# Optimization experiments

Hardware: AMD Instinct MI355X
Metric: run time of the kernel (lower is better)

Reference implementation:

```python
import jax, jax.numpy as jnp
import numpy as np

N_NODES = 50000
IN_CH = 256
Z_DIM = 64
N_EDGES = 800000


def setup_inputs() -> dict:
    key = jax.random.key(0)
    k_x, k_e, k_wm, k_ws = jax.random.split(key, 4)
    x = jax.random.normal(k_x, (N_NODES, IN_CH), dtype=jnp.float32)
    edge_index = jax.random.randint(k_e, (2, N_EDGES), 0, N_NODES, dtype=jnp.int64)
    # Glorot-style init like PyG GCNConv
    scale = 1.0 / np.sqrt(IN_CH)
    W_mu = jax.random.uniform(k_wm, (IN_CH, Z_DIM), dtype=jnp.float32, minval=-scale, maxval=scale)
    W_logstd = jax.random.uniform(k_ws, (IN_CH, Z_DIM), dtype=jnp.float32, minval=-scale, maxval=scale)
    b_mu = jnp.zeros((Z_DIM,), dtype=jnp.float32)
    b_logstd = jnp.zeros((Z_DIM,), dtype=jnp.float32)
    return {"x": x, "edge_index": edge_index, "W_mu": W_mu, "b_mu": b_mu,
            "W_logstd": W_logstd, "b_logstd": b_logstd}


def _gcn_conv(x, W, b, src, dst, deg_inv_sqrt, num_nodes):
    # PyG GCNConv: out = D^{-1/2} (A + I) D^{-1/2} X W + b
    xw = x @ W                                   # [N, Z]
    norm = deg_inv_sqrt[src] * deg_inv_sqrt[dst]  # [E+N]
    msg = xw[src] * norm[:, None]                 # gather + scale, [E+N, Z]
    agg = jax.ops.segment_sum(msg, dst, num_segments=num_nodes)  # scatter-add
    return agg + b


def reference(x, edge_index, W_mu, b_mu, W_logstd, b_logstd):
    num_nodes = x.shape[0]
    loops = jnp.arange(num_nodes, dtype=edge_index.dtype)
    src = jnp.concatenate([edge_index[0], loops])
    dst = jnp.concatenate([edge_index[1], loops])
    # degree (with self loops) on target nodes, symmetric normalization
    deg = jax.ops.segment_sum(jnp.ones_like(dst, dtype=x.dtype), dst, num_segments=num_nodes)
    deg_inv_sqrt = jnp.where(deg > 0, jax.lax.rsqrt(jnp.maximum(deg, 1.0)), 0.0)
    mu = _gcn_conv(x, W_mu, b_mu, src, dst, deg_inv_sqrt, num_nodes)
    logstd = _gcn_conv(x, W_logstd, b_logstd, src, dst, deg_inv_sqrt, num_nodes)
    return (mu, logstd)
```

## Files before the change

kernel.cpp:

```cpp
#include <hip/hip_runtime.h>

#define N_NODES 50000
#define IN_CH   256
#define Z_DIM   64
#define N_EDGES 800000
#define CH2     128
#define NODE_OFF (N_NODES * Z_DIM)
#define NBLK    ((N_NODES + 255) / 256)
#define SEG     8
#define NBUCKET (SEG * N_NODES)
#define CAP     16
#define ECHUNKS (N_EDGES / 256)
#define NTILES  ((N_NODES + 31) / 32)
#define NW      32768

typedef __bf16 bf16x8 __attribute__((ext_vector_type(8)));
typedef float  f32x4  __attribute__((ext_vector_type(4)));

__device__ __forceinline__ unsigned short f2bf(float f) {
    __bf16 h = (__bf16)f;
    unsigned short u;
    __builtin_memcpy(&u, &h, 2);
    return u;
}
__device__ __forceinline__ float bf_lo(unsigned w) { return __uint_as_float(w << 16); }
__device__ __forceinline__ float bf_hi(unsigned w) { return __uint_as_float(w & 0xFFFF0000u); }

__global__ void k_pre(int* __restrict__ cur8,
                      const float* __restrict__ Wmu, const float* __restrict__ Wls,
                      unsigned short* __restrict__ WbT) {
    int g = blockIdx.x * 256 + threadIdx.x;
    if (g < NBUCKET) cur8[g] = 0;
    int h = g - NBUCKET;
    if (h >= 0 && h < NW) {
        int n = h >> 8, k = h & 255;
        float v = (n < 64) ? Wmu[(size_t)k * 64 + n] : Wls[(size_t)k * 64 + (n - 64)];
        WbT[(size_t)n * 256 + k] = f2bf(v);
    }
}

#define LDP  264
#define CSP2 136
__device__ __forceinline__ void gemm_tile(int t, const float* __restrict__ x,
                                          const unsigned short* __restrict__ WbT,
                                          unsigned short* __restrict__ xwb, char* smem) {
    unsigned short* As  = (unsigned short*)smem;
    unsigned short* Css = (unsigned short*)smem;
    const int tid = threadIdx.x;
    const int r0  = t * 32;

    {
        int row_l = tid >> 3;
        int cb    = (tid & 7) * 32;
        int row   = r0 + row_l;
        unsigned short* dp = As + row_l * LDP + cb;
        if (row < N_NODES) {
            const float4* xp = (const float4*)(x + (size_t)row * IN_CH + cb);
#pragma unroll
            for (int i = 0; i < 4; ++i) {
                float4 a = xp[2 * i];
                float4 b = xp[2 * i + 1];
                uint4 w;
                w.x = (unsigned)f2bf(a.x) | ((unsigned)f2bf(a.y) << 16);
                w.y = (unsigned)f2bf(a.z) | ((unsigned)f2bf(a.w) << 16);
                w.z = (unsigned)f2bf(b.x) | ((unsigned)f2bf(b.y) << 16);
                w.w = (unsigned)f2bf(b.z) | ((unsigned)f2bf(b.w) << 16);
                *(uint4*)(dp + i * 8) = w;
            }
        } else {
            uint4 z = make_uint4(0, 0, 0, 0);
#pragma unroll
            for (int i = 0; i < 4; ++i) *(uint4*)(dp + i * 8) = z;
        }
    }
    __syncthreads();

    const int wv   = tid >> 6;
    const int lane = tid & 63;
    const int m    = lane & 15;
    const int q    = lane >> 4;
    const int row_half = (wv & 1) * 16;
    const int col_half = (wv >> 1) * 64;

    f32x4 acc[4] = {};
    const unsigned short* ap = As + (row_half + m) * LDP + q * 8;
    const unsigned short* bp = WbT + (size_t)(col_half + m) * 256 + q * 8;

#pragma unroll
    for (int k0 = 0; k0 < IN_CH; k0 += 32) {
        bf16x8 af = *(const bf16x8*)(ap + k0);
#pragma unroll
        for (int nt = 0; nt < 4; ++nt) {
            bf16x8 bf_ = *(const bf16x8*)(bp + (size_t)nt * 16 * 256 + k0);
            acc[nt] = __builtin_amdgcn_mfma_f32_16x16x32_bf16(af, bf_, acc[nt], 0, 0, 0);
        }
    }

    __syncthreads();
#pragma unroll
    for (int nt = 0; nt < 4; ++nt)
#pragma unroll
        for (int r = 0; r < 4; ++r)
            Css[(row_half + q * 4 + r) * CSP2 + col_half + nt * 16 + m] = f2bf(acc[nt][r]);
    __syncthreads();

    {
        int row_l = tid >> 3;
        int c0    = (tid & 7) * 16;
        int row   = r0 + row_l;
        if (row < N_NODES) {
            const uint4* cp = (const uint4*)(Css + row_l * CSP2 + c0);
            uint4 w0 = cp[0];
            uint4 w1 = cp[1];
            uint4* op = (uint4*)(xwb + (size_t)row * CH2 + c0);
            op[0] = w0;
            op[1] = w1;
        }
    }
    __syncthreads();
}

__global__ __launch_bounds__(256) void k_gemm_scat(
    const float* __restrict__ x, const unsigned short* __restrict__ WbT,
    unsigned short* __restrict__ xwb,
    const int* __restrict__ src, const int* __restrict__ dst,
    int* __restrict__ cur8, unsigned short* __restrict__ pk2) {
    __shared__ __align__(16) char smem[32 * LDP * 2];
    if (blockIdx.x < NTILES) {
        gemm_tile(blockIdx.x, x, WbT, xwb, smem);
    } else {
        int c = blockIdx.x - NTILES;
        int e = c * 256 + threadIdx.x;
        int s = src[e];
        int d = dst[e];
        int seg = c & (SEG - 1);
        int idx = seg * N_NODES + d;
        int pos = atomicAdd(&cur8[idx], 1);
        if (pos < CAP) pk2[(size_t)idx * CAP + pos] = (unsigned short)s;
    }
}

__global__ void k_dinv(const int* __restrict__ cur8, float* __restrict__ dinv) {
    int i = blockIdx.x * 256 + threadIdx.x;
    if (i >= N_NODES) return;
    int t = 1;
#pragma unroll
    for (int xg = 0; xg < SEG; ++xg) t += cur8[xg * N_NODES + i];
    dinv[i] = rsqrtf((float)t);
}

__global__ __launch_bounds__(256) void k_gather(const int* __restrict__ cur8,
                                                const unsigned short* __restrict__ pk2,
                                                const unsigned short* __restrict__ xwb,
                                                const float* __restrict__ dinv,
                                                const float* __restrict__ bmu,
                                                const float* __restrict__ bls,
                                                float* __restrict__ out) {
    const int i    = blockIdx.x * 4 + (threadIdx.x >> 6);
    const int lane = threadIdx.x & 63;
    const int q    = lane >> 4;
    const int cl   = lane & 15;

    float di = dinv[i];
    float acc[8] = {0.f, 0.f, 0.f, 0.f, 0.f, 0.f, 0.f, 0.f};
    if (q == 0) {
        float sq = di * di;
        uint4 w = *(const uint4*)(xwb + (size_t)i * CH2 + cl * 8);
        acc[0] = bf_lo(w.x) * sq; acc[1] = bf_hi(w.x) * sq;
        acc[2] = bf_lo(w.y) * sq; acc[3] = bf_hi(w.y) * sq;
        acc[4] = bf_lo(w.z) * sq; acc[5] = bf_hi(w.z) * sq;
        acc[6] = bf_lo(w.w) * sq; acc[7] = bf_hi(w.w) * sq;
    }

#pragma unroll
    for (int b = 0; b < 2; ++b) {
        int idx = (q + b * 4) * N_NODES + i;
        int cnt = cur8[idx];
        if (cnt > CAP) cnt = CAP;
        size_t base = (size_t)idx * CAP;
        for (int j = 0; j < cnt; ++j) {
            int s = pk2[base + j];
            float nrm = di * dinv[s];
            uint4 w = *(const uint4*)(xwb + (size_t)s * CH2 + cl * 8);
            acc[0] += bf_lo(w.x) * nrm; acc[1] += bf_hi(w.x) * nrm;
            acc[2] += bf_lo(w.y) * nrm; acc[3] += bf_hi(w.y) * nrm;
            acc[4] += bf_lo(w.z) * nrm; acc[5] += bf_hi(w.z) * nrm;
            acc[6] += bf_lo(w.w) * nrm; acc[7] += bf_hi(w.w) * nrm;
        }
    }

#pragma unroll
    for (int k = 0; k < 8; ++k) {
        acc[k] += __shfl_xor(acc[k], 16);
        acc[k] += __shfl_xor(acc[k], 32);
    }

    if (lane < 16) {
        int c0 = cl * 8;
        const float* bb = (c0 < 64) ? (bmu + c0) : (bls + (c0 - 64));
        float4 b0 = *(const float4*)(bb + 0);
        float4 b1 = *(const float4*)(bb + 4);
        float* o = (c0 < 64) ? (out + (size_t)i * 64 + c0)
                             : (out + NODE_OFF + (size_t)i * 64 + (c0 - 64));
        *(float4*)(o + 0) = make_float4(acc[0] + b0.x, acc[1] + b0.y,
                                        acc[2] + b0.z, acc[3] + b0.w);
        *(float4*)(o + 4) = make_float4(acc[4] + b1.x, acc[5] + b1.y,
                                        acc[6] + b1.z, acc[7] + b1.w);
    }
}

extern "C" void kernel_launch(void* const* d_in, const int* in_sizes, int n_in,
                              void* d_out, int out_size, void* d_ws, size_t ws_size,
                              hipStream_t stream) {
    const float* x   = (const float*)d_in[0];
    const int*   ei  = (const int*)d_in[1];
    const float* Wmu = (const float*)d_in[2];
    const float* bmu = (const float*)d_in[3];
    const float* Wls = (const float*)d_in[4];
    const float* bls = (const float*)d_in[5];
    float* out = (float*)d_out;

    const int* src = ei;
    const int* dst = ei + N_EDGES;

    char* ws = (char*)d_ws;
    int*            cur8 = (int*)(ws + 0);
    float*          dinv = (float*)(ws + 1638400);
    unsigned short* WbT  = (unsigned short*)(ws + 1867776);
    unsigned short* pk2  = (unsigned short*)(ws + 2097152);
    unsigned short* xwb  = (unsigned short*)(ws + 16777216);

    k_pre<<<(NBUCKET + NW + 255) / 256, 256, 0, stream>>>(cur8, Wmu, Wls, WbT);
    k_gemm_scat<<<NTILES + ECHUNKS, 256, 0, stream>>>(x, WbT, xwb, src, dst, cur8, pk2);
    k_dinv<<<NBLK, 256, 0, stream>>>(cur8, dinv);
    k_gather<<<N_NODES / 4, 256, 0, stream>>>(cur8, pk2, xwb, dinv, bmu, bls, out);
}
```

Measured before the change: 227.3 us.

## Bucket edges by XCC with workgroup-scope atomics and unroll gather with vector index loads

```diff
diff --git a/kernel.cpp b/kernel.cpp
--- a/kernel.cpp
+++ b/kernel.cpp
@@ -8,7 +8,8 @@
 #define NODE_OFF (N_NODES * Z_DIM)
 #define NBLK    ((N_NODES + 255) / 256)
 #define SEG     8
-#define NBUCKET (SEG * N_NODES)
+#define SEGN    50048
+#define NBUCKET (SEG * SEGN)
 #define CAP     16
 #define ECHUNKS (N_EDGES / 256)
 #define NTILES  ((N_NODES + 31) / 32)
@@ -133,9 +134,12 @@
         int e = c * 256 + threadIdx.x;
         int s = src[e];
         int d = dst[e];
-        int seg = c & (SEG - 1);
-        int idx = seg * N_NODES + d;
-        int pos = atomicAdd(&cur8[idx], 1);
+        unsigned xcc;
+        asm("s_getreg_b32 %0, hwreg(HW_REG_XCC_ID)" : "=s"(xcc));
+        int seg = (int)(xcc & (SEG - 1));
+        int idx = seg * SEGN + d;
+        int pos = __hip_atomic_fetch_add(&cur8[idx], 1, __ATOMIC_RELAXED,
+                                         __HIP_MEMORY_SCOPE_WORKGROUP);
         if (pos < CAP) pk2[(size_t)idx * CAP + pos] = (unsigned short)s;
     }
 }
@@ -145,9 +149,29 @@
     if (i >= N_NODES) return;
     int t = 1;
 #pragma unroll
-    for (int xg = 0; xg < SEG; ++xg) t += cur8[xg * N_NODES + i];
+    for (int xg = 0; xg < SEG; ++xg) t += cur8[xg * SEGN + i];
     dinv[i] = rsqrtf((float)t);
 }
+
+#define PAIR(jj, pr)                                                          \
+    if (2 * (jj) < cnt) {                                                     \
+        int sa = (int)((pr) & 0xFFFFu);                                       \
+        int sb = (int)((pr) >> 16);                                           \
+        bool hb = (2 * (jj) + 1) < cnt;                                       \
+        int sbe = hb ? sb : sa;                                               \
+        float na = di * dinv[sa];                                             \
+        float nb = hb ? di * dinv[sbe] : 0.f;                                 \
+        const uint4 wa = *(const uint4*)(xwb + (size_t)sa * CH2 + cl * 8);    \
+        const uint4 wb = *(const uint4*)(xwb + (size_t)sbe * CH2 + cl * 8);   \
+        acc[0] += bf_lo(wa.x) * na + bf_lo(wb.x) * nb;                        \
+        acc[1] += bf_hi(wa.x) * na + bf_hi(wb.x) * nb;                        \
+        acc[2] += bf_lo(wa.y) * na + bf_lo(wb.y) * nb;                        \
+        acc[3] += bf_hi(wa.y) * na + bf_hi(wb.y) * nb;                        \
+        acc[4] += bf_lo(wa.z) * na + bf_lo(wb.z) * nb;                        \
+        acc[5] += bf_hi(wa.z) * na + bf_hi(wb.z) * nb;                        \
+        acc[6] += bf_lo(wa.w) * na + bf_lo(wb.w) * nb;                        \
+        acc[7] += bf_hi(wa.w) * na + bf_hi(wb.w) * nb;                        \
+    }
 
 __global__ __launch_bounds__(256) void k_gather(const int* __restrict__ cur8,
                                                 const unsigned short* __restrict__ pk2,
@@ -174,19 +198,14 @@
 
 #pragma unroll
     for (int b = 0; b < 2; ++b) {
-        int idx = (q + b * 4) * N_NODES + i;
+        const int idx = (q + b * 4) * SEGN + i;
         int cnt = cur8[idx];
         if (cnt > CAP) cnt = CAP;
-        size_t base = (size_t)idx * CAP;
-        for (int j = 0; j < cnt; ++j) {
-            int s = pk2[base + j];
-            float nrm = di * dinv[s];
-            uint4 w = *(const uint4*)(xwb + (size_t)s * CH2 + cl * 8);
-            acc[0] += bf_lo(w.x) * nrm; acc[1] += bf_hi(w.x) * nrm;
-            acc[2] += bf_lo(w.y) * nrm; acc[3] += bf_hi(w.y) * nrm;
-            acc[4] += bf_lo(w.z) * nrm; acc[5] += bf_hi(w.z) * nrm;
-            acc[6] += bf_lo(w.w) * nrm; acc[7] += bf_hi(w.w) * nrm;
-        }
+        const uint4* pb = (const uint4*)(pk2 + (size_t)idx * CAP);
+        const uint4 e0 = pb[0];
+        const uint4 e1 = pb[1];
+        PAIR(0, e0.x) PAIR(1, e0.y) PAIR(2, e0.z) PAIR(3, e0.w)
+        PAIR(4, e1.x) PAIR(5, e1.y) PAIR(6, e1.z) PAIR(7, e1.w)
     }
 
 #pragma unroll
```

New measurement: 211.2 us. 7.1% less time.
